# Kernel optimization log

Hardware: AMD Instinct MI355X
Metric: run time of the kernel (lower is better)

Reference implementation:

```python
import math
import jax, jax.numpy as jnp
import numpy as np


def positional_encoding(c, h, w):
    # Faithful port of the torch positional_encode grid (c divisible by 4).
    half = c // 2
    div = jnp.exp(jnp.arange(0, half, 2, dtype=jnp.float32) * (-math.log(10000.0) / half))  # [half/2]
    pos_w = jnp.arange(w, dtype=jnp.float32)[:, None]  # [w,1]
    pos_h = jnp.arange(h, dtype=jnp.float32)[:, None]  # [h,1]
    q = half // 2
    pe = jnp.zeros((c, h, w), dtype=jnp.float32)
    sw = jnp.sin(pos_w * div).T[:, None, :]  # [q,1,w] -> broadcast over height
    cw = jnp.cos(pos_w * div).T[:, None, :]
    sh = jnp.sin(pos_h * div).T[:, :, None]  # [q,h,1] -> broadcast over width
    ch = jnp.cos(pos_h * div).T[:, :, None]
    pe = pe.at[0:half:2].set(jnp.broadcast_to(sw, (q, h, w)))
    pe = pe.at[1:half:2].set(jnp.broadcast_to(cw, (q, h, w)))
    pe = pe.at[half::2].set(jnp.broadcast_to(sh, (q, h, w)))
    pe = pe.at[half + 1::2].set(jnp.broadcast_to(ch, (q, h, w)))
    return pe


def setup_inputs() -> dict:
    key = jax.random.key(0)
    k1, k2, k3, k4 = jax.random.split(key, 4)
    b, c, h, w = 4, 256, 64, 64
    x = jax.random.normal(k1, (b, c, h, w), dtype=jnp.float32)
    # kaiming_uniform-ish scale for d x d weights
    bound = 1.0 / math.sqrt(c)
    Wq = jax.random.uniform(k2, (c, c), dtype=jnp.float32, minval=-bound, maxval=bound)
    Wk = jax.random.uniform(k3, (c, c), dtype=jnp.float32, minval=-bound, maxval=bound)
    Wv = jax.random.uniform(k4, (c, c), dtype=jnp.float32, minval=-bound, maxval=bound)
    return {"x": x, "Wq": Wq, "Wk": Wk, "Wv": Wv}


def reference(x, Wq, Wk, Wv):
    b, c, h, w = x.shape
    pe = positional_encoding(c, h, w)
    xt = (x + pe).reshape(b, c, h * w).transpose(0, 2, 1)  # [b, hw, c]
    Q = xt @ Wq  # [b, hw, c]
    K = xt @ Wk
    V = xt @ Wv
    scores = jnp.einsum('bqc,bkc->bqk', Q, K) / math.sqrt(c)  # [b, hw, hw]
    # NOTE: softmax over dim=1 (the QUERY axis), matching nn.Softmax(dim=1)
    A = jax.nn.softmax(scores, axis=1)
    out = jnp.einsum('bqk,bkc->bqc', A, V)  # [b, hw, c]
    return out.transpose(0, 2, 1).reshape(b, c, h, w)
```

## Files before the change

### kernel.cpp

```cpp
#include <hip/hip_runtime.h>
#include <hip/hip_bf16.h>
#include <math.h>

typedef float f32x4 __attribute__((ext_vector_type(4)));
typedef short bf16x8 __attribute__((ext_vector_type(8)));
typedef short bf16x4 __attribute__((ext_vector_type(4)));

#define AS1 __attribute__((address_space(1)))
#define AS3 __attribute__((address_space(3)))

__device__ __forceinline__ short f2bf(float f) {
    unsigned u = __float_as_uint(f);
    unsigned r = (u + 0x7fffu + ((u >> 16) & 1u)) >> 16;
    return (short)r;
}
__device__ __forceinline__ float bf2f(short s) {
    return __uint_as_float(((unsigned)(unsigned short)s) << 16);
}
__device__ __forceinline__ void gld16(const void* g, void* l) {
    __builtin_amdgcn_global_load_lds((const AS1 unsigned int*)g, (AS3 unsigned int*)l, 16, 0, 0);
}

__device__ __forceinline__ void stage128x64(const short* __restrict__ g,
                                            short* lds, int t) {
    int w = t >> 6, l = t & 63;
    #pragma unroll
    for (int j = 0; j < 4; ++j) {
        int ii = j * 4 + w;
        int row = ii * 8 + (l >> 3);
        int slot = (l & 7) ^ (row & 7);
        gld16(g + row * 256 + slot * 8, lds + ii * 512);
    }
}

__device__ __forceinline__ void stage64x64(const short* __restrict__ g,
                                           short* lds, int t) {
    #pragma unroll
    for (int j = 0; j < 2; ++j) {
        int idx = j * 256 + t;
        int row = idx >> 3;
        int slot = (idx & 7) ^ (row & 7);
        gld16(g + (size_t)row * 4096 + slot * 8, lds + idx * 8);
    }
}

__device__ __forceinline__ void stage128x64v(const short* __restrict__ g,
                                             short* lds, int t) {
    #pragma unroll
    for (int j = 0; j < 4; ++j) {
        int idx = j * 256 + t;
        int row = idx >> 3;
        int slot = (idx & 7) ^ (row & 7);
        gld16(g + (size_t)row * 4096 + slot * 8, lds + idx * 8);
    }
}

__global__ __launch_bounds__(256) void k_prep(const float* __restrict__ x,
                                              const float* __restrict__ Wq,
                                              const float* __restrict__ Wk,
                                              const float* __restrict__ Wv,
                                              short* __restrict__ xt,
                                              short* __restrict__ Wt) {
    int bidx = blockIdx.x;
    if (bidx < 768) {
        int wsel = bidx >> 8, n = bidx & 255, k = threadIdx.x;
        const float* W = (wsel == 0) ? Wq : (wsel == 1) ? Wk : Wv;
        Wt[(wsel * 256 + n) * 256 + k] = f2bf(W[k * 256 + n]);
        return;
    }
    int bid = bidx - 768;
    int b = bid >> 7;
    int pb = bid & 127;
    __shared__ __align__(16) float tile[256][33];
    __shared__ __align__(16) float pew[128][32];
    __shared__ __align__(16) float peh[128];
    int t = threadIdx.x;
    const float c1 = 0.14391156f;
    int wbase = (pb & 1) * 32;
    int hpos = pb >> 1;
    #pragma unroll
    for (int j = 0; j < 16; ++j) {
        int idx = t + j * 256;
        int c = idx >> 5, pp = idx & 31;
        int i = c >> 1;
        float d = expf(-(float)i * c1);
        float arg = (float)(wbase + pp) * d;
        pew[c][pp] = (c & 1) ? cosf(arg) : sinf(arg);
    }
    if (t < 128) {
        int i = t >> 1;
        float d = expf(-(float)i * c1);
        float arg = (float)hpos * d;
        peh[t] = (t & 1) ? cosf(arg) : sinf(arg);
    }
    int p0 = pb * 32;
    #pragma unroll
    for (int j = 0; j < 32; ++j) {
        int c = j * 8 + (t >> 5);
        int pp = t & 31;
        tile[c][pp] = x[((b * 256 + c) << 12) + p0 + pp];
    }
    __syncthreads();
    int pp = t >> 3, cseg = t & 7;
    int p = p0 + pp;
    short* dst = xt + (((b << 12) + p) << 8) + (cseg << 5);
    #pragma unroll
    for (int j = 0; j < 4; ++j) {
        bf16x8 v;
        #pragma unroll
        for (int e = 0; e < 8; ++e) {
            int c = cseg * 32 + j * 8 + e;
            float pe = (c < 128) ? pew[c][pp] : peh[c - 128];
            v[e] = f2bf(tile[c][pp] + pe);
        }
        ((bf16x8*)dst)[j] = v;
    }
}

__global__ __launch_bounds__(256) void k_proj(const short* __restrict__ xt,
                                              const short* __restrict__ Wt,
                                              short* __restrict__ Q,
                                              short* __restrict__ K,
                                              short* __restrict__ VT) {
    int id = blockIdx.x;
    int wsel = id % 3; id /= 3;
    int nt = id & 1;  id >>= 1;
    int mt = id & 31; int b = id >> 5;
    int t = threadIdx.x, l = t & 63, w = t >> 6;
    int lr = l & 15, lg = l >> 4;
    int m0 = mt * 128 + (w >> 1) * 64;
    int n0 = nt * 128 + (w & 1) * 64;
    const short* wbase = Wt + wsel * 65536;
    f32x4 acc[4][4] = {};
    #pragma unroll
    for (int s = 0; s < 8; ++s) {
        bf16x8 af[4], bw[4];
        #pragma unroll
        for (int ms = 0; ms < 4; ++ms)
            af[ms] = *(const bf16x8*)(xt + ((b << 12) + m0 + ms * 16 + lr) * 256 + s * 32 + lg * 8);
        #pragma unroll
        for (int fn = 0; fn < 4; ++fn)
            bw[fn] = *(const bf16x8*)(wbase + (n0 + fn * 16 + lr) * 256 + s * 32 + lg * 8);
        #pragma unroll
        for (int ms = 0; ms < 4; ++ms)
            #pragma unroll
            for (int fn = 0; fn < 4; ++fn)
                acc[ms][fn] = __builtin_amdgcn_mfma_f32_16x16x32_bf16(af[ms], bw[fn], acc[ms][fn], 0, 0, 0);
    }
    if (wsel < 2) {
        float scl = (wsel == 0) ? 0.0625f : 1.0f;
        short* dst = (wsel == 0) ? Q : K;
        #pragma unroll
        for (int ms = 0; ms < 4; ++ms)
            #pragma unroll
            for (int fn = 0; fn < 4; ++fn)
                #pragma unroll
                for (int r = 0; r < 4; ++r) {
                    int m = m0 + ms * 16 + lg * 4 + r;
                    int n = n0 + fn * 16 + lr;
                    dst[((b << 12) + m) * 256 + n] = f2bf(acc[ms][fn][r] * scl);
                }
    } else {
        #pragma unroll
        for (int ms = 0; ms < 4; ++ms)
            #pragma unroll
            for (int fn = 0; fn < 4; ++fn) {
                int n = n0 + fn * 16 + lr;
                int m = m0 + ms * 16 + lg * 4;
                bf16x4 v;
                #pragma unroll
                for (int r = 0; r < 4; ++r) v[r] = f2bf(acc[ms][fn][r]);
                *(bf16x4*)(VT + ((b * 256 + n) << 12) + m) = v;
            }
    }
}

__global__ __launch_bounds__(256, 4) void k_E(const short* __restrict__ Qm,
                                              const short* __restrict__ Km,
                                              short* __restrict__ E,
                                              float* __restrict__ pl) {
    int o = blockIdx.x;
    int bid = (o & 7) * 512 + (o >> 3);
    int qt = bid & 31, kt = (bid >> 5) & 31, b = bid >> 10;
    int t = threadIdx.x, l = t & 63;
    int w = t >> 6;
    int wr = w >> 1, wc = w & 1;
    int lr = l & 15, lg = l >> 4;
    __shared__ __align__(16) short Ka[128 * 64];
    __shared__ __align__(16) short Qa[128 * 64];
    __shared__ float plds[128];
    const short* Kg = Km + (((size_t)b << 12) + kt * 128) * 256;
    const short* Qg = Qm + (((size_t)b << 12) + qt * 128) * 256;
    f32x4 acc[4][4] = {};

    #pragma unroll
    for (int ks = 0; ks < 4; ++ks) {
        stage128x64(Kg + ks * 64, Ka, t);
        stage128x64(Qg + ks * 64, Qa, t);
        __syncthreads();
        #pragma unroll
        for (int s = 0; s < 2; ++s) {
            bf16x8 a[4], bq[4];
            #pragma unroll
            for (int mk = 0; mk < 4; ++mk) {
                int row = wr * 64 + mk * 16 + lr;
                a[mk] = *(const bf16x8*)(Ka + row * 64 + (((s * 4 + lg) ^ (row & 7)) << 3));
            }
            #pragma unroll
            for (int nq = 0; nq < 4; ++nq) {
                int row = wc * 64 + nq * 16 + lr;
                bq[nq] = *(const bf16x8*)(Qa + row * 64 + (((s * 4 + lg) ^ (row & 7)) << 3));
            }
            #pragma unroll
            for (int mk = 0; mk < 4; ++mk)
                #pragma unroll
                for (int nq = 0; nq < 4; ++nq)
                    acc[mk][nq] = __builtin_amdgcn_mfma_f32_16x16x32_bf16(a[mk], bq[nq], acc[mk][nq], 0, 0, 0);
        }
        __syncthreads();
    }

    int k0 = kt * 128 + wr * 64;
    int q0 = qt * 128 + wc * 64;
    float psum[4][4];
    #pragma unroll
    for (int mk = 0; mk < 4; ++mk) {
        float ps0 = 0.f, ps1 = 0.f, ps2 = 0.f, ps3 = 0.f;
        #pragma unroll
        for (int nq = 0; nq < 4; ++nq) {
            int q = q0 + nq * 16 + lr;
            float e0 = __expf(acc[mk][nq][0]);
            float e1 = __expf(acc[mk][nq][1]);
            float e2 = __expf(acc[mk][nq][2]);
            float e3 = __expf(acc[mk][nq][3]);
            ps0 += e0; ps1 += e1; ps2 += e2; ps3 += e3;
            bf16x4 ev;
            ev[0] = f2bf(e0); ev[1] = f2bf(e1); ev[2] = f2bf(e2); ev[3] = f2bf(e3);
            *(bf16x4*)(E + (((size_t)b << 12) + q) * 4096 + k0 + mk * 16 + lg * 4) = ev;
        }
        psum[mk][0] = ps0; psum[mk][1] = ps1; psum[mk][2] = ps2; psum[mk][3] = ps3;
    }
    #pragma unroll
    for (int mk = 0; mk < 4; ++mk)
        #pragma unroll
        for (int r = 0; r < 4; ++r) {
            float v = psum[mk][r];
            v += __shfl_xor(v, 1);
            v += __shfl_xor(v, 2);
            v += __shfl_xor(v, 4);
            v += __shfl_xor(v, 8);
            psum[mk][r] = v;
        }
    if (wc == 0 && lr == 0) {
        #pragma unroll
        for (int mk = 0; mk < 4; ++mk)
            #pragma unroll
            for (int r = 0; r < 4; ++r)
                plds[wr * 64 + mk * 16 + lg * 4 + r] = psum[mk][r];
    }
    __syncthreads();
    if (wc == 1 && lr == 0) {
        #pragma unroll
        for (int mk = 0; mk < 4; ++mk)
            #pragma unroll
            for (int r = 0; r < 4; ++r)
                plds[wr * 64 + mk * 16 + lg * 4 + r] += psum[mk][r];
    }
    __syncthreads();
    if (t < 128) pl[(b * 32 + qt) * 4096 + kt * 128 + t] = plds[t];
}

__global__ void k_lred(const float* __restrict__ pl, float* __restrict__ rl) {
    int gid = blockIdx.x * 256 + threadIdx.x;
    float s = 0.f;
    int b = gid >> 12, k = gid & 4095;
    #pragma unroll
    for (int qt = 0; qt < 32; ++qt) s += pl[(b * 32 + qt) * 4096 + k];
    rl[gid] = 1.0f / s;
}

__global__ void k_vn(const short* __restrict__ VT, const float* __restrict__ rl,
                     short* __restrict__ Vnt) {
    int gid = blockIdx.x * 256 + threadIdx.x;
    int idx8 = gid * 8;
    int b = idx8 >> 20;
    int rem = idx8 & 1048575;
    int k = rem & 4095;
    bf16x8 v = *(const bf16x8*)(VT + idx8);
    const float* rb = rl + (b << 12) + k;
    f32x4 r0 = *(const f32x4*)(rb);
    f32x4 r1 = *(const f32x4*)(rb + 4);
    bf16x8 oo;
    #pragma unroll
    for (int e = 0; e < 8; ++e) {
        float f = bf2f(v[e]);
        float rr = (e < 4) ? r0[e] : r1[e - 4];
        oo[e] = f2bf(f * rr);
    }
    *(bf16x8*)(Vnt + idx8) = oo;
}

__global__ __launch_bounds__(256) void k_pv(const short* __restrict__ E,
                                            const short* __restrict__ Vnt,
                                            float* __restrict__ out) {
    int o = blockIdx.x;
    int ct = o >> 8;
    int r = o & 255;
    int b = r >> 6, qt = r & 63;
    int t = threadIdx.x, l = t & 63, w = t >> 6;
    int wq = w >> 1, wc = w & 1;
    int lr = l & 15, lg = l >> 4;
    int q0 = qt * 64, c0 = ct * 128;
    __shared__ __align__(16) short Ea[64 * 64];
    __shared__ __align__(16) short Va[128 * 64];
    const short* Eg = E + (((size_t)b << 12) + q0) * 4096;
    const short* Vg = Vnt + ((size_t)(b * 256 + c0)) * 4096;
    f32x4 acc[2][4] = {};

    for (int kc = 0; kc < 4096; kc += 64) {
        stage64x64(Eg + kc, Ea, t);
        stage128x64v(Vg + kc, Va, t);
        __syncthreads();
        bf16x8 Af[2][2], Bf[4][2];
        #pragma unroll
        for (int s = 0; s < 2; ++s) {
            #pragma unroll
            for (int mq = 0; mq < 2; ++mq) {
                int row = wq * 32 + mq * 16 + lr;
                Af[mq][s] = *(const bf16x8*)(Ea + row * 64 + (((s * 4 + lg) ^ (row & 7)) << 3));
            }
            #pragma unroll
            for (int nc = 0; nc < 4; ++nc) {
                int row = wc * 64 + nc * 16 + lr;
                Bf[nc][s] = *(const bf16x8*)(Va + row * 64 + (((s * 4 + lg) ^ (row & 7)) << 3));
            }
        }
        #pragma unroll
        for (int s = 0; s < 2; ++s)
            #pragma unroll
            for (int mq = 0; mq < 2; ++mq)
                #pragma unroll
                for (int nc = 0; nc < 4; ++nc)
                    acc[mq][nc] = __builtin_amdgcn_mfma_f32_16x16x32_bf16(Af[mq][s], Bf[nc][s], acc[mq][nc], 0, 0, 0);
        __syncthreads();
    }
    #pragma unroll
    for (int mq = 0; mq < 2; ++mq)
        #pragma unroll
        for (int nc = 0; nc < 4; ++nc) {
            int c = c0 + wc * 64 + nc * 16 + lr;
            int q = q0 + wq * 32 + mq * 16 + lg * 4;
            *(f32x4*)(out + (((size_t)b << 8) + c) * 4096 + q) = acc[mq][nc];
        }
}

extern "C" void kernel_launch(void* const* d_in, const int* in_sizes, int n_in,
                              void* d_out, int out_size, void* d_ws, size_t ws_size,
                              hipStream_t stream) {
    const float* x  = (const float*)d_in[0];
    const float* Wq = (const float*)d_in[1];
    const float* Wk = (const float*)d_in[2];
    const float* Wv = (const float*)d_in[3];

    char* p = (char*)d_ws;
    short* xt  = (short*)p; p += 4 * 4096 * 256 * 2;
    short* Wt  = (short*)p; p += 3 * 256 * 256 * 2;
    short* Qm  = (short*)p; p += 4 * 4096 * 256 * 2;
    short* Km  = (short*)p; p += 4 * 4096 * 256 * 2;
    short* VT  = (short*)p; p += 4 * 4096 * 256 * 2;
    short* E   = (short*)p; p += (size_t)4 * 4096 * 4096 * 2;
    float* pl  = (float*)p; p += 4 * 32 * 4096 * 4;
    float* rl  = (float*)p; p += 4 * 4096 * 4;
    short* Vnt = (short*)p; p += 4 * 4096 * 256 * 2;

    float* out = (float*)d_out;

    k_prep <<<1280, 256, 0, stream>>>(x, Wq, Wk, Wv, xt, Wt);
    k_proj <<<768, 256, 0, stream>>>(xt, Wt, Qm, Km, VT);
    k_E    <<<4096, 256, 0, stream>>>(Qm, Km, E, pl);
    k_lred <<<64,   256, 0, stream>>>(pl, rl);
    k_vn   <<<2048, 256, 0, stream>>>(VT, rl, Vnt);
    k_pv   <<<512,  256, 0, stream>>>(E, Vnt, out);
}
```

Measured before the change: 176.9 us.

## Stage projection operands through swizzled LDS tiles via async global-to-LDS loads

The QKV projection kernel now stages 128x64 tiles of X and W into shared memory with the existing stage128x64 helper (global_load_lds) over four K-steps, instead of each wave loading its MFMA fragments straight from global memory. Fragments are read from LDS with an XOR swizzle to avoid bank conflicts. This lets the two waves sharing rows or columns reuse the staged data and cuts redundant global traffic. Launch bounds now request 4 blocks per CU. The cost is 32 KB of LDS per block plus two barriers per K-step, with no double buffering.

After: 164.7 us (median of 3 runs). 1.07x faster.

```diff
diff --git a/kernel.cpp b/kernel.cpp
--- a/kernel.cpp
+++ b/kernel.cpp
@@ -117,36 +117,53 @@
     }
 }
 
-__global__ __launch_bounds__(256) void k_proj(const short* __restrict__ xt,
-                                              const short* __restrict__ Wt,
-                                              short* __restrict__ Q,
-                                              short* __restrict__ K,
-                                              short* __restrict__ VT) {
+__global__ __launch_bounds__(256, 4) void k_proj(const short* __restrict__ xt,
+                                                 const short* __restrict__ Wt,
+                                                 short* __restrict__ Q,
+                                                 short* __restrict__ K,
+                                                 short* __restrict__ VT) {
     int id = blockIdx.x;
     int wsel = id % 3; id /= 3;
     int nt = id & 1;  id >>= 1;
     int mt = id & 31; int b = id >> 5;
     int t = threadIdx.x, l = t & 63, w = t >> 6;
     int lr = l & 15, lg = l >> 4;
-    int m0 = mt * 128 + (w >> 1) * 64;
-    int n0 = nt * 128 + (w & 1) * 64;
-    const short* wbase = Wt + wsel * 65536;
+    int wr = w >> 1, wc = w & 1;
+    __shared__ __align__(16) short Xa[128 * 64];
+    __shared__ __align__(16) short Wa[128 * 64];
+    const short* Xg = xt + (((size_t)b << 12) + mt * 128) * 256;
+    const short* Wg = Wt + ((size_t)wsel * 256 + nt * 128) * 256;
     f32x4 acc[4][4] = {};
-    #pragma unroll
-    for (int s = 0; s < 8; ++s) {
-        bf16x8 af[4], bw[4];
-        #pragma unroll
-        for (int ms = 0; ms < 4; ++ms)
-            af[ms] = *(const bf16x8*)(xt + ((b << 12) + m0 + ms * 16 + lr) * 256 + s * 32 + lg * 8);
-        #pragma unroll
-        for (int fn = 0; fn < 4; ++fn)
-            bw[fn] = *(const bf16x8*)(wbase + (n0 + fn * 16 + lr) * 256 + s * 32 + lg * 8);
-        #pragma unroll
-        for (int ms = 0; ms < 4; ++ms)
-            #pragma unroll
-            for (int fn = 0; fn < 4; ++fn)
-                acc[ms][fn] = __builtin_amdgcn_mfma_f32_16x16x32_bf16(af[ms], bw[fn], acc[ms][fn], 0, 0, 0);
-    }
+
+    #pragma unroll
+    for (int ks = 0; ks < 4; ++ks) {
+        stage128x64(Xg + ks * 64, Xa, t);
+        stage128x64(Wg + ks * 64, Wa, t);
+        __syncthreads();
+        #pragma unroll
+        for (int s = 0; s < 2; ++s) {
+            bf16x8 af[4], bw[4];
+            #pragma unroll
+            for (int ms = 0; ms < 4; ++ms) {
+                int row = wr * 64 + ms * 16 + lr;
+                af[ms] = *(const bf16x8*)(Xa + row * 64 + (((s * 4 + lg) ^ (row & 7)) << 3));
+            }
+            #pragma unroll
+            for (int fn = 0; fn < 4; ++fn) {
+                int row = wc * 64 + fn * 16 + lr;
+                bw[fn] = *(const bf16x8*)(Wa + row * 64 + (((s * 4 + lg) ^ (row & 7)) << 3));
+            }
+            #pragma unroll
+            for (int ms = 0; ms < 4; ++ms)
+                #pragma unroll
+                for (int fn = 0; fn < 4; ++fn)
+                    acc[ms][fn] = __builtin_amdgcn_mfma_f32_16x16x32_bf16(af[ms], bw[fn], acc[ms][fn], 0, 0, 0);
+        }
+        __syncthreads();
+    }
+
+    int m0 = mt * 128 + wr * 64;
+    int n0 = nt * 128 + wc * 64;
     if (wsel < 2) {
         float scl = (wsel == 0) ? 0.0625f : 1.0f;
         short* dst = (wsel == 0) ? Q : K;
```
